# Optimization experiments

Measured on AMD Instinct MI355X. Metric: run time of the kernel, lower is better.

## Reference

```python
import jax, jax.numpy as jnp
import numpy as np

EPS = 1e-5
K_GROUP = 8  # k_group_size


def setup_inputs() -> dict:
    key = jax.random.key(0)
    ks = jax.random.split(key, 8)
    C = 384  # encoder_channel
    rn = lambda k, s: (jax.random.normal(k, s, dtype=jnp.float32) * 0.05)
    return {
        "point_groups": jax.random.normal(ks[0], (4, 256, 32, 3), dtype=jnp.float32),
        # first_conv: Conv1d(3,128,1)+BN+ReLU+Conv1d(128,256,1)
        "W1": rn(ks[1], (128, 3)), "b1": jnp.zeros(128, jnp.float32),
        "gamma1": jnp.ones(128, jnp.float32), "beta1": jnp.zeros(128, jnp.float32),
        "W2": rn(ks[2], (256, 128)), "b2": jnp.zeros(256, jnp.float32),
        # second_conv: Conv1d(512,512,1)+BN+ReLU+Conv1d(512,C,1)
        "W3": rn(ks[3], (512, 512)), "b3": jnp.zeros(512, jnp.float32),
        "gamma3": jnp.ones(512, jnp.float32), "beta3": jnp.zeros(512, jnp.float32),
        "W4": rn(ks[4], (C, 512)), "b4": jnp.zeros(C, jnp.float32),
        # K_Norm affine (out_dim = C, matching declared parameter shapes)
        "alpha": jnp.ones((1, 1, 1, C), jnp.float32),
        "beta_aff": jnp.zeros((1, 1, 1, C), jnp.float32),
        # fusion_layer: Conv1d(2C,C,1)+BN+ReLU
        "Wf": rn(ks[5], (C, 2 * C)), "bf": jnp.zeros(C, jnp.float32),
        "gammaf": jnp.ones(C, jnp.float32), "betaf": jnp.zeros(C, jnp.float32),
    }


def _conv1x1(x, W, b):  # x: (B,Cin,L), W: (Cout,Cin)
    return jnp.einsum("bcl,oc->bol", x, W) + b[None, :, None]


def _bn(x, gamma, beta):  # training-mode BatchNorm1d over (batch, length)
    mu = jnp.mean(x, axis=(0, 2), keepdims=True)
    var = jnp.var(x, axis=(0, 2), keepdims=True)
    xh = (x - mu) * jax.lax.rsqrt(var + EPS)
    return xh * gamma[None, :, None] + beta[None, :, None]


def reference(point_groups, W1, b1, gamma1, beta1, W2, b2, W3, b3, gamma3, beta3,
              W4, b4, alpha, beta_aff, Wf, bf, gammaf, betaf):
    bs, g, n, _ = point_groups.shape
    C = W4.shape[0]
    pg = point_groups.reshape(bs * g, n, 3)  # (B', n, 3)

    # first_conv stack
    f = _conv1x1(pg.transpose(0, 2, 1), W1, b1)           # (B',128,n)
    f = jax.nn.relu(_bn(f, gamma1, beta1))
    f = _conv1x1(f, W2, b2)                               # (B',256,n)
    fg = jnp.max(f, axis=2, keepdims=True)                # (B',256,1)
    f = jnp.concatenate([jnp.broadcast_to(fg, f.shape), f], axis=1)  # (B',512,n)

    # second_conv stack
    f = _conv1x1(f, W3, b3)
    f = jax.nn.relu(_bn(f, gamma3, beta3))
    f = _conv1x1(f, W4, b4)                               # (B',C,n)
    feat = f.transpose(0, 2, 1)                           # (B',n,C)

    # KNN within each group (self included, as in KNN(xyz,xyz))
    sq = jnp.sum(pg * pg, axis=-1)                        # (B',n)
    d = sq[:, :, None] + sq[:, None, :] - 2.0 * jnp.einsum("bnc,bmc->bnm", pg, pg)
    _, idx = jax.lax.top_k(-d, K_GROUP)                   # (B',n,K)

    gather = jax.vmap(lambda a, i: a[i])
    knn_x = gather(feat, idx)                             # (B',n,K,C)

    # K_Norm: center-relative normalization by global scalar std (torch.std, ddof=1)
    mean_x = feat[:, :, None, :]
    dx = knn_x - mean_x
    std_x = jnp.std(dx, ddof=1)
    knn_x = dx / (std_x + EPS)
    knn_x = alpha * knn_x + beta_aff                      # (B',n,K,C)

    enhanced = jnp.mean(knn_x, axis=2)                    # mean over K -> (B',n,C)
    enhanced = jnp.mean(enhanced, axis=1)                 # pool over n -> (B',C)

    fg2 = jnp.max(f, axis=2)                              # (B',C)
    fused_in = jnp.concatenate([fg2, enhanced], axis=1)[:, :, None]  # (B',2C,1)
    fused = jax.nn.relu(_bn(_conv1x1(fused_in, Wf, bf), gammaf, betaf))[:, :, 0]
    return fused.reshape(bs, g, C)
```

## Files before the change

### kernel.cpp

```cpp
#include <hip/hip_runtime.h>
#include <math.h>

#define EPS 1e-5f

typedef __attribute__((ext_vector_type(8))) short s16x8;
typedef __attribute__((ext_vector_type(4))) float f32x4;

__device__ __forceinline__ unsigned short f2bf(float x) {
    unsigned u = __float_as_uint(x);
    u += 0x7fffu + ((u >> 16) & 1u);
    return (unsigned short)(u >> 16);
}
__device__ __forceinline__ float bf2f(unsigned short h) {
    return __uint_as_float(((unsigned)h) << 16);
}
__device__ __forceinline__ unsigned long long pack4bf(float a, float b, float c, float d) {
    return (unsigned long long)f2bf(a)
         | ((unsigned long long)f2bf(b) << 16)
         | ((unsigned long long)f2bf(c) << 32)
         | ((unsigned long long)f2bf(d) << 48);
}

template<int CTRL>
__device__ __forceinline__ float dppmov(float x) {
    return __int_as_float(__builtin_amdgcn_update_dpp(
        0, __float_as_int(x), CTRL, 0xF, 0xF, true));
}
__device__ __forceinline__ float red16_sum(float x) {
    x += dppmov<0xB1>(x);
    x += dppmov<0x4E>(x);
    x += dppmov<0x141>(x);
    x += dppmov<0x140>(x);
    return x;
}
__device__ __forceinline__ float red16_max(float x) {
    x = fmaxf(x, dppmov<0xB1>(x));
    x = fmaxf(x, dppmov<0x4E>(x));
    x = fmaxf(x, dppmov<0x141>(x));
    x = fmaxf(x, dppmov<0x140>(x));
    return x;
}

__global__ __launch_bounds__(128) void k1_conv1_knn(
    const float* __restrict__ pg, const float* __restrict__ W1,
    const float* __restrict__ b1,
    const float* __restrict__ W2, const float* __restrict__ W3,
    const float* __restrict__ W4, const float* __restrict__ Wf,
    unsigned short* __restrict__ h1b, float* __restrict__ p1s, float* __restrict__ p1q,
    int* __restrict__ idxw,
    unsigned short* __restrict__ W2b, unsigned short* __restrict__ W3b,
    unsigned short* __restrict__ W4b, unsigned short* __restrict__ Wfb)
{
    __shared__ float pgs[96];
    __shared__ float sqs[32];
    if (blockIdx.x >= 1024) {
        const int i = (blockIdx.x - 1024) * 128 + threadIdx.x;
        if (i < 32768)  W2b[i] = f2bf(W2[i]);
        if (i < 262144) W3b[i] = f2bf(W3[i]);
        if (i < 196608) W4b[i] = f2bf(W4[i]);
        if (i < 294912) Wfb[i] = f2bf(Wf[i]);
        return;
    }
    const int b = blockIdx.x;
    const int t = threadIdx.x;
    if (t < 96) pgs[t] = pg[b * 96 + t];
    __syncthreads();
    if (t < 32) {
        float x = pgs[t*3+0], y = pgs[t*3+1], z = pgs[t*3+2];
        sqs[t] = x*x + y*y + z*z;
    }
    __syncthreads();
    {
        const float w0 = W1[t*3+0], w1 = W1[t*3+1], w2 = W1[t*3+2];
        const float bb = b1[t];
        float s = 0.f, q = 0.f;
        unsigned short* hcol = h1b + (size_t)b*4096 + t;
        #pragma unroll
        for (int l = 0; l < 32; ++l) {
            float v = fmaf(w2, pgs[l*3+2], fmaf(w1, pgs[l*3+1], fmaf(w0, pgs[l*3+0], bb)));
            hcol[l*128] = f2bf(v); s += v; q += v*v;
        }
        p1s[b*128 + t] = s;
        p1q[b*128 + t] = q;
    }
    if (t < 32) {
        const float xl = pgs[t*3+0], yl = pgs[t*3+1], zl = pgs[t*3+2];
        const float sql = sqs[t];
        float dist[32];
        #pragma unroll
        for (int m = 0; m < 32; ++m) {
            float dot = xl*pgs[m*3+0] + yl*pgs[m*3+1] + zl*pgs[m*3+2];
            dist[m] = sql + sqs[m] - 2.f*dot;
        }
        unsigned used = 0u;
        int* orow = idxw + b*256 + t*8;
        #pragma unroll
        for (int j = 0; j < 8; ++j) {
            float best = 3.4e38f; int bi = 0;
            #pragma unroll
            for (int m = 0; m < 32; ++m) {
                if (!((used >> m) & 1u) && dist[m] < best) { best = dist[m]; bi = m; }
            }
            used |= (1u << bi);
            orow[j] = bi;
        }
    }
}

__global__ __launch_bounds__(256) void k_bn_fin2(
    const float* __restrict__ ps, const float* __restrict__ pq,
    int nPart, int nChan, float invN,
    const float* __restrict__ gamma, const float* __restrict__ beta,
    float* __restrict__ scale, float* __restrict__ shift)
{
    const int ob = blockIdx.x * 4;
    const int t = threadIdx.x;
    const int co = t & 3, i0 = t >> 2;
    float s = 0.f, q = 0.f;
    for (int i = i0; i < nPart; i += 64) {
        s += ps[(size_t)i*nChan + ob + co];
        q += pq[(size_t)i*nChan + ob + co];
    }
    #pragma unroll
    for (int off = 32; off >= 4; off >>= 1) {
        s += __shfl_down(s, off, 64);
        q += __shfl_down(q, off, 64);
    }
    __shared__ float ss[4][4], qs[4][4];
    const int wid = t >> 6, lane = t & 63;
    if (lane < 4) { ss[wid][lane] = s; qs[wid][lane] = q; }
    __syncthreads();
    if (t < 4) {
        float S = ss[0][t] + ss[1][t] + ss[2][t] + ss[3][t];
        float Q = qs[0][t] + qs[1][t] + qs[2][t] + qs[3][t];
        const int o = ob + t;
        float mu  = S * invN;
        float var = Q * invN - mu*mu;
        float sc  = gamma[o] * rsqrtf(var + EPS);
        scale[o] = sc;
        shift[o] = beta[o] - mu * sc;
    }
}

__global__ __launch_bounds__(512, 4) void k3_mfma(
    const unsigned short* __restrict__ h1b,
    const float* __restrict__ scale1, const float* __restrict__ shift1,
    const unsigned short* __restrict__ W2b, const float* __restrict__ b2,
    const unsigned short* __restrict__ W3b, const float* __restrict__ b3,
    unsigned short* __restrict__ h3b, float* __restrict__ p3s, float* __restrict__ p3q)
{
    const int g0 = blockIdx.x * 2;
    const int t = threadIdx.x;
    __shared__ __align__(16) unsigned short SB[26128];
    unsigned short* B1  = SB;
    unsigned short* F2  = SB + 8704;
    unsigned short* FGB = SB + 25600;

    {
        const int l = t >> 3, c0 = (t & 7) * 16;
        const int g = g0 + (l >> 5);
        #pragma unroll
        for (int h = 0; h < 2; ++h) {
            s16x8 hv = *(const s16x8*)(h1b + (size_t)g*4096 + (l & 31)*128 + c0 + h*8);
            unsigned short ov[8];
            #pragma unroll
            for (int e = 0; e < 8; ++e) {
                int c = c0 + h*8 + e;
                float v = fmaxf(fmaf(bf2f((unsigned short)hv[e]), scale1[c], shift1[c]), 0.f);
                ov[e] = f2bf(v);
            }
            uint4 o4;
            o4.x = (unsigned)ov[0] | ((unsigned)ov[1] << 16);
            o4.y = (unsigned)ov[2] | ((unsigned)ov[3] << 16);
            o4.z = (unsigned)ov[4] | ((unsigned)ov[5] << 16);
            o4.w = (unsigned)ov[6] | ((unsigned)ov[7] << 16);
            *(uint4*)&B1[l*136 + c0 + h*8] = o4;
        }
    }
    __syncthreads();

    const int wave = t >> 6;
    const int lane = t & 63;
    const int m    = lane & 15;
    const int quad = lane >> 4;

    f32x4 acc2[2][4];
    #pragma unroll
    for (int mt = 0; mt < 2; ++mt)
        #pragma unroll
        for (int n = 0; n < 4; ++n)
            acc2[mt][n] = (f32x4){0.f, 0.f, 0.f, 0.f};

    #pragma unroll
    for (int kt = 0; kt < 4; ++kt) {
        s16x8 bv[4];
        #pragma unroll
        for (int nt = 0; nt < 4; ++nt)
            bv[nt] = *(const s16x8*)&B1[(nt*16 + m)*136 + kt*32 + quad*8];
        #pragma unroll
        for (int mt = 0; mt < 2; ++mt) {
            s16x8 av = *(const s16x8*)(W2b + (size_t)(wave*32 + mt*16 + m)*128 + kt*32 + quad*8);
            #pragma unroll
            for (int nt = 0; nt < 4; ++nt)
                acc2[mt][nt] = __builtin_amdgcn_mfma_f32_16x16x32_bf16(av, bv[nt], acc2[mt][nt], 0, 0, 0);
        }
    }

    #pragma unroll
    for (int mt = 0; mt < 2; ++mt) {
        const int o0 = wave*32 + mt*16 + quad*4;
        #pragma unroll
        for (int r = 0; r < 4; ++r) {
            float bb = b2[o0 + r];
            #pragma unroll
            for (int nt = 0; nt < 4; ++nt) acc2[mt][nt][r] += bb;
        }
        #pragma unroll
        for (int nt = 0; nt < 4; ++nt) {
            const int row = nt*16 + m;
            *(unsigned long long*)&F2[row*264 + o0] =
                pack4bf(acc2[mt][nt][0], acc2[mt][nt][1], acc2[mt][nt][2], acc2[mt][nt][3]);
        }
        float f0[4], f1[4];
        #pragma unroll
        for (int r = 0; r < 4; ++r) {
            f0[r] = red16_max(fmaxf(acc2[mt][0][r], acc2[mt][1][r]));
            f1[r] = red16_max(fmaxf(acc2[mt][2][r], acc2[mt][3][r]));
        }
        if (m == 0) {
            *(unsigned long long*)&FGB[o0]       = pack4bf(f0[0], f0[1], f0[2], f0[3]);
            *(unsigned long long*)&FGB[264 + o0] = pack4bf(f1[0], f1[1], f1[2], f1[3]);
        }
    }
    __syncthreads();

    f32x4 facc[4];
    #pragma unroll
    for (int i = 0; i < 4; ++i) facc[i] = (f32x4){0.f, 0.f, 0.f, 0.f};
    #pragma unroll
    for (int kt = 0; kt < 8; ++kt) {
        s16x8 bg = *(const s16x8*)&FGB[(m & 1)*264 + kt*32 + quad*8];
        #pragma unroll
        for (int i = 0; i < 4; ++i) {
            s16x8 av = *(const s16x8*)(W3b + (size_t)((wave*4 + i)*16 + m)*512 + kt*32 + quad*8);
            facc[i] = __builtin_amdgcn_mfma_f32_16x16x32_bf16(av, bg, facc[i], 0, 0, 0);
        }
    }

    f32x4 acc3[4][4];
    #pragma unroll
    for (int mt = 0; mt < 4; ++mt) {
        #pragma unroll
        for (int r = 0; r < 4; ++r) {
            const int ob = (wave*4 + mt)*16 + quad*4 + r;
            float self = facc[mt][r];
            float oth  = dppmov<0xB1>(self);
            float fg_g0 = (m & 1) ? oth : self;
            float fg_g1 = (m & 1) ? self : oth;
            float bb = b3[ob];
            acc3[mt][0][r] = bb + fg_g0;
            acc3[mt][1][r] = bb + fg_g0;
            acc3[mt][2][r] = bb + fg_g1;
            acc3[mt][3][r] = bb + fg_g1;
        }
    }
    #pragma unroll 4
    for (int kt = 0; kt < 8; ++kt) {
        s16x8 bv[4];
        #pragma unroll
        for (int nt = 0; nt < 4; ++nt)
            bv[nt] = *(const s16x8*)&F2[(nt*16 + m)*264 + kt*32 + quad*8];
        #pragma unroll
        for (int mt = 0; mt < 4; ++mt) {
            s16x8 av = *(const s16x8*)(W3b + (size_t)((wave*4 + mt)*16 + m)*512 + 256 + kt*32 + quad*8);
            #pragma unroll
            for (int nt = 0; nt < 4; ++nt)
                acc3[mt][nt] = __builtin_amdgcn_mfma_f32_16x16x32_bf16(av, bv[nt], acc3[mt][nt], 0, 0, 0);
        }
    }

    unsigned short* dst = h3b + (size_t)blockIdx.x * 32768;
    #pragma unroll
    for (int mt = 0; mt < 4; ++mt) {
        const int ot = wave*4 + mt;
        const int o0 = ot*16 + quad*4;
        float s[4], q[4];
        #pragma unroll
        for (int r = 0; r < 4; ++r) {
            float x0 = acc3[mt][0][r], x1 = acc3[mt][1][r];
            float x2 = acc3[mt][2][r], x3 = acc3[mt][3][r];
            s[r] = (x0 + x1) + (x2 + x3);
            q[r] = (x0*x0 + x1*x1) + (x2*x2 + x3*x3);
        }
        {
            unsigned long long u0 = pack4bf(acc3[mt][0][0], acc3[mt][0][1], acc3[mt][0][2], acc3[mt][0][3]);
            unsigned long long u1 = pack4bf(acc3[mt][1][0], acc3[mt][1][1], acc3[mt][1][2], acc3[mt][1][3]);
            unsigned long long u2 = pack4bf(acc3[mt][2][0], acc3[mt][2][1], acc3[mt][2][2], acc3[mt][2][3]);
            unsigned long long u3 = pack4bf(acc3[mt][3][0], acc3[mt][3][1], acc3[mt][3][2], acc3[mt][3][3]);
            unsigned short* p = dst + (size_t)(ot*64 + lane) * 16;
            *(uint4*)(p)     = make_uint4((unsigned)u0, (unsigned)(u0 >> 32), (unsigned)u1, (unsigned)(u1 >> 32));
            *(uint4*)(p + 8) = make_uint4((unsigned)u2, (unsigned)(u2 >> 32), (unsigned)u3, (unsigned)(u3 >> 32));
        }
        #pragma unroll
        for (int r = 0; r < 4; ++r) {
            s[r] = red16_sum(s[r]);
            q[r] = red16_sum(q[r]);
        }
        if (m == 0) {
            #pragma unroll
            for (int r = 0; r < 4; ++r) {
                p3s[(size_t)blockIdx.x*512 + o0 + r] = s[r];
                p3q[(size_t)blockIdx.x*512 + o0 + r] = q[r];
            }
        }
    }
}

__global__ __launch_bounds__(512, 4) void k5_mfma(
    const unsigned short* __restrict__ h3b,
    const float* __restrict__ scale3, const float* __restrict__ shift3,
    const unsigned short* __restrict__ W4b, const float* __restrict__ b4,
    const int* __restrict__ idxw,
    float* __restrict__ fg2, float* __restrict__ A,
    float* __restrict__ S1p, float* __restrict__ S2p)
{
    const int g0 = blockIdx.x * 2;
    const int t = threadIdx.x;
    __shared__ __align__(16) unsigned short SB[33280];
    unsigned short* B4 = SB;
    unsigned short* XT = SB;
    unsigned short* Mm = SB + 30720;
    __shared__ int icnt[2][32];
    __shared__ float r1[2][8], r2[2][8];

    {
        const uint4* src = (const uint4*)(h3b + (size_t)blockIdx.x * 32768);
        for (int i = t; i < 4096; i += 512) {
            uint4 hv = src[i];
            const int flat16 = i >> 1, half = i & 1;
            const int ln = flat16 & 63, m2 = ln & 15, q2 = ln >> 4;
            const int wm = flat16 >> 6;
            const int o0 = wm*16 + q2*4;
            const float4 sc = *(const float4*)(scale3 + o0);
            const float4 sh = *(const float4*)(shift3 + o0);
            const int rowa = (half*2)*16 + m2;
            float a0 = fmaxf(fmaf(bf2f((unsigned short)(hv.x       )), sc.x, sh.x), 0.f);
            float a1 = fmaxf(fmaf(bf2f((unsigned short)(hv.x >> 16 )), sc.y, sh.y), 0.f);
            float a2 = fmaxf(fmaf(bf2f((unsigned short)(hv.y       )), sc.z, sh.z), 0.f);
            float a3 = fmaxf(fmaf(bf2f((unsigned short)(hv.y >> 16 )), sc.w, sh.w), 0.f);
            float b0 = fmaxf(fmaf(bf2f((unsigned short)(hv.z       )), sc.x, sh.x), 0.f);
            float b1 = fmaxf(fmaf(bf2f((unsigned short)(hv.z >> 16 )), sc.y, sh.y), 0.f);
            float b2 = fmaxf(fmaf(bf2f((unsigned short)(hv.w       )), sc.z, sh.z), 0.f);
            float b3 = fmaxf(fmaf(bf2f((unsigned short)(hv.w >> 16 )), sc.w, sh.w), 0.f);
            *(unsigned long long*)&B4[rowa*520 + o0]        = pack4bf(a0, a1, a2, a3);
            *(unsigned long long*)&B4[(rowa + 16)*520 + o0] = pack4bf(b0, b1, b2, b3);
        }
    }
    if (t < 64) icnt[t >> 5][t & 31] = 0;
    __syncthreads();

    const int wave = t >> 6;
    const int lane = t & 63;
    const int m    = lane & 15;
    const int quad = lane >> 4;

    f32x4 acc4[3][4];
    #pragma unroll
    for (int mt = 0; mt < 3; ++mt)
        #pragma unroll
        for (int n = 0; n < 4; ++n)
            acc4[mt][n] = (f32x4){0.f, 0.f, 0.f, 0.f};

    #pragma unroll 4
    for (int kt = 0; kt < 16; ++kt) {
        s16x8 bv[4];
        #pragma unroll
        for (int nt = 0; nt < 4; ++nt)
            bv[nt] = *(const s16x8*)&B4[(nt*16 + m)*520 + kt*32 + quad*8];
        #pragma unroll
        for (int mt = 0; mt < 3; ++mt) {
            s16x8 av = *(const s16x8*)(W4b + (size_t)(wave*48 + mt*16 + m)*512 + kt*32 + quad*8);
            #pragma unroll
            for (int nt = 0; nt < 4; ++nt)
                acc4[mt][nt] = __builtin_amdgcn_mfma_f32_16x16x32_bf16(av, bv[nt], acc4[mt][nt], 0, 0, 0);
        }
    }

    #pragma unroll
    for (int mt = 0; mt < 3; ++mt) {
        const int o0 = wave*48 + mt*16 + quad*4;
        float f0[4], f1[4];
        #pragma unroll
        for (int r = 0; r < 4; ++r) {
            float bb = b4[o0 + r];
            #pragma unroll
            for (int nt = 0; nt < 4; ++nt) acc4[mt][nt][r] += bb;
            f0[r] = red16_max(fmaxf(acc4[mt][0][r], acc4[mt][1][r]));
            f1[r] = red16_max(fmaxf(acc4[mt][2][r], acc4[mt][3][r]));
        }
        if (m == 0) {
            #pragma unroll
            for (int r = 0; r < 4; ++r) {
                fg2[(size_t)g0*384 + o0 + r]     = f0[r];
                fg2[(size_t)(g0+1)*384 + o0 + r] = f1[r];
            }
        }
    }
    __syncthreads();

    #pragma unroll
    for (int mt = 0; mt < 3; ++mt) {
        const int o0 = wave*48 + mt*16 + quad*4;
        #pragma unroll
        for (int nt = 0; nt < 4; ++nt) {
            const int g = nt >> 1;
            const int l = (nt & 1)*16 + m;
            unsigned short* xg = XT + g*15360;
            #pragma unroll
            for (int r = 0; r < 4; ++r)
                xg[(o0 + r)*40 + l] = f2bf(acc4[mt][nt][r]);
        }
    }
    if (t < 64) {
        const int g = t >> 5, l = t & 31;
        uint4 z = make_uint4(0u, 0u, 0u, 0u);
        #pragma unroll
        for (int i = 0; i < 5; ++i)
            *(uint4*)&Mm[g*1280 + l*40 + i*8] = z;
    }
    __syncthreads();

    if (t < 64) {
        const int g = t >> 5, l = t & 31;
        const int* ip = idxw + (size_t)(g0 + g)*256 + l*8;
        #pragma unroll
        for (int j = 0; j < 8; ++j) {
            int ix = ip[j];
            Mm[g*1280 + l*40 + ix] = 0x3F80;
            atomicAdd(&icnt[g][ix], 1);
        }
    }
    __syncthreads();

    float s1loc[2] = {0.f, 0.f}, s2loc[2] = {0.f, 0.f};
    #pragma unroll
    for (int g = 0; g < 2; ++g) {
        const float c0 = (float)icnt[g][m];
        const float c1 = (float)icnt[g][m + 16];
        const float w0 = c0 - 8.f, u0 = c0 + 8.f;
        const float w1 = c1 - 8.f, u1 = c1 + 8.f;
        #pragma unroll
        for (int mt = 0; mt < 3; ++mt) {
            const int o0 = wave*48 + mt*16 + quad*4;
            float Ap[4];
            #pragma unroll
            for (int r = 0; r < 4; ++r) {
                const float x0 = acc4[mt][g*2 + 0][r];
                const float x1 = acc4[mt][g*2 + 1][r];
                Ap[r] = w0*x0 + w1*x1;
                s1loc[g] += Ap[r];
                s2loc[g] += u0*x0*x0 + u1*x1*x1;
            }
            #pragma unroll
            for (int r = 0; r < 4; ++r)
                Ap[r] = red16_sum(Ap[r]);
            if (m == 0) {
                #pragma unroll
                for (int r = 0; r < 4; ++r)
                    A[(size_t)(g0 + g)*384 + o0 + r] = Ap[r];
            }
        }
    }

    #pragma unroll
    for (int g = 0; g < 2; ++g) {
        const unsigned short* xg = XT + g*15360;
        float cross = 0.f;
        #pragma unroll
        for (int lt = 0; lt < 2; ++lt) {
            s16x8 af = *(const s16x8*)&Mm[g*1280 + (lt*16 + m)*40 + quad*8];
            #pragma unroll
            for (int i = 0; i < 3; ++i) {
                const int oc = (wave*3 + i)*16 + m;
                s16x8 bfv = *(const s16x8*)&xg[oc*40 + quad*8];
                f32x4 sa = __builtin_amdgcn_mfma_f32_16x16x32_bf16(
                    af, bfv, (f32x4){0.f, 0.f, 0.f, 0.f}, 0, 0, 0);
                #pragma unroll
                for (int r = 0; r < 4; ++r) {
                    const int lp = lt*16 + quad*4 + r;
                    cross = fmaf(bf2f(xg[oc*40 + lp]), sa[r], cross);
                }
            }
        }
        s2loc[g] -= 2.f * cross;
    }

    #pragma unroll
    for (int g = 0; g < 2; ++g) {
        float sA = s1loc[g], sQ = s2loc[g];
        #pragma unroll
        for (int off = 32; off > 0; off >>= 1) {
            sA += __shfl_down(sA, off, 64);
            sQ += __shfl_down(sQ, off, 64);
        }
        if (lane == 0) { r1[g][wave] = sA; r2[g][wave] = sQ; }
    }
    __syncthreads();
    if (t < 2) {
        float S = 0.f, Q = 0.f;
        #pragma unroll
        for (int w = 0; w < 8; ++w) { S += r1[t][w]; Q += r2[t][w]; }
        S1p[g0 + t] = S;
        S2p[g0 + t] = Q;
    }
}

__global__ __launch_bounds__(384) void k7_fused(
    const float* __restrict__ fg2, const float* __restrict__ A,
    const float* __restrict__ alpha, const float* __restrict__ beta_aff,
    const float* __restrict__ S1p, const float* __restrict__ S2p,
    const unsigned short* __restrict__ Wfb, const float* __restrict__ bf,
    float* __restrict__ hf, float* __restrict__ pfs, float* __restrict__ pfq)
{
    const int blk    = blockIdx.x;
    const int slice  = blk >> 2;
    const int msplit = blk & 3;
    const int g0     = slice * 16;
    const int obase  = msplit * 96;
    const int t = threadIdx.x;
    __shared__ __align__(16) char smem[24832];
    unsigned short* xfb = (unsigned short*)smem;
    float* OTf = (float*)smem;
    __shared__ double rs[6], rq[6];
    __shared__ float stdsh;

    {
        double s = 0.0, q = 0.0;
        for (int i = t; i < 1024; i += 384) { s += (double)S1p[i]; q += (double)S2p[i]; }
        #pragma unroll
        for (int off = 32; off > 0; off >>= 1) {
            s += __shfl_down(s, off, 64);
            q += __shfl_down(q, off, 64);
        }
        if ((t & 63) == 0) { rs[t >> 6] = s; rq[t >> 6] = q; }
        __syncthreads();
        if (t == 0) {
            double S = 0.0, Q = 0.0;
            #pragma unroll
            for (int w = 0; w < 6; ++w) { S += rs[w]; Q += rq[w]; }
            const double N = 1024.0 * 32.0 * 8.0 * 384.0;
            double var = (Q - S*S/N) / (N - 1.0);
            stdsh = (float)sqrt(var);
        }
        __syncthreads();
    }
    const float inv = 1.f / (256.f * (stdsh + EPS));

    for (int i = t; i < 16*96; i += 384) {
        const int row = i / 96, c8 = (i % 96) * 8;
        const int g = g0 + row;
        float e[8];
        if (c8 < 384) {
            const float4* s0 = (const float4*)(fg2 + (size_t)g*384 + c8);
            float4 v0 = s0[0], v1 = s0[1];
            e[0]=v0.x; e[1]=v0.y; e[2]=v0.z; e[3]=v0.w;
            e[4]=v1.x; e[5]=v1.y; e[6]=v1.z; e[7]=v1.w;
        } else {
            const int cc = c8 - 384;
            const float4* s0 = (const float4*)(A + (size_t)g*384 + cc);
            float4 v0 = s0[0], v1 = s0[1];
            float av[8] = {v0.x,v0.y,v0.z,v0.w,v1.x,v1.y,v1.z,v1.w};
            #pragma unroll
            for (int j = 0; j < 8; ++j)
                e[j] = fmaf(alpha[cc+j] * inv, av[j], beta_aff[cc+j]);
        }
        uint4 o4;
        o4.x = (unsigned)f2bf(e[0]) | ((unsigned)f2bf(e[1]) << 16);
        o4.y = (unsigned)f2bf(e[2]) | ((unsigned)f2bf(e[3]) << 16);
        o4.z = (unsigned)f2bf(e[4]) | ((unsigned)f2bf(e[5]) << 16);
        o4.w = (unsigned)f2bf(e[6]) | ((unsigned)f2bf(e[7]) << 16);
        *(uint4*)&xfb[row*776 + c8] = o4;
    }
    __syncthreads();

    const int wave = t >> 6;
    const int lane = t & 63;
    const int m    = lane & 15;
    const int quad = lane >> 4;

    f32x4 acc = (f32x4){0.f, 0.f, 0.f, 0.f};
    #pragma unroll 4
    for (int kt = 0; kt < 24; ++kt) {
        s16x8 bv = *(const s16x8*)&xfb[m*776 + kt*32 + quad*8];
        s16x8 av = *(const s16x8*)(Wfb + (size_t)(obase + wave*16 + m)*768 + kt*32 + quad*8);
        acc = __builtin_amdgcn_mfma_f32_16x16x32_bf16(av, bv, acc, 0, 0, 0);
    }

    {
        const int o0 = obase + wave*16 + quad*4;
        float s[4], q[4];
        #pragma unroll
        for (int r = 0; r < 4; ++r) {
            acc[r] += bf[o0 + r];
            s[r] = red16_sum(acc[r]);
            q[r] = red16_sum(acc[r]*acc[r]);
        }
        if (m == 0) {
            #pragma unroll
            for (int r = 0; r < 4; ++r) {
                pfs[(size_t)slice*384 + o0 + r] = s[r];
                pfq[(size_t)slice*384 + o0 + r] = q[r];
            }
        }
    }
    __syncthreads();

    {
        const int lo0 = wave*16 + quad*4;
        #pragma unroll
        for (int r = 0; r < 4; ++r)
            OTf[m*100 + lo0 + r] = acc[r];
    }
    __syncthreads();

    {
        const int grp = t / 24, c4 = t % 24;
        float4 v = *(const float4*)&OTf[grp*100 + c4*4];
        *(float4*)(hf + (size_t)(g0 + grp)*384 + obase + c4*4) = v;
    }
}

__global__ __launch_bounds__(384) void k9_out(
    const float* __restrict__ hf,
    const float* __restrict__ pfs, const float* __restrict__ pfq,
    const float* __restrict__ gammaf, const float* __restrict__ betaf,
    float* __restrict__ out)
{
    const int blk = blockIdx.x, t = threadIdx.x;
    float S = 0.f, Q = 0.f;
    #pragma unroll 8
    for (int i = 0; i < 64; ++i) {
        S += pfs[(size_t)i*384 + t];
        Q += pfq[(size_t)i*384 + t];
    }
    const float mu  = S * (1.f/1024.f);
    const float var = Q * (1.f/1024.f) - mu*mu;
    const float sc  = gammaf[t] * rsqrtf(var + EPS);
    const float sh  = betaf[t] - mu * sc;
    const size_t base = (size_t)blk * 8 * 384;
    #pragma unroll
    for (int g = 0; g < 8; ++g) {
        float v = fmaf(hf[base + g*384 + t], sc, sh);
        out[base + g*384 + t] = fmaxf(v, 0.f);
    }
}

extern "C" void kernel_launch(void* const* d_in, const int* in_sizes, int n_in,
                              void* d_out, int out_size, void* d_ws, size_t ws_size,
                              hipStream_t stream) {
    const float* pg      = (const float*)d_in[0];
    const float* W1      = (const float*)d_in[1];
    const float* b1      = (const float*)d_in[2];
    const float* gamma1  = (const float*)d_in[3];
    const float* beta1   = (const float*)d_in[4];
    const float* W2      = (const float*)d_in[5];
    const float* b2      = (const float*)d_in[6];
    const float* W3      = (const float*)d_in[7];
    const float* b3      = (const float*)d_in[8];
    const float* gamma3  = (const float*)d_in[9];
    const float* beta3   = (const float*)d_in[10];
    const float* W4      = (const float*)d_in[11];
    const float* b4      = (const float*)d_in[12];
    const float* alpha   = (const float*)d_in[13];
    const float* beta_af = (const float*)d_in[14];
    const float* Wf      = (const float*)d_in[15];
    const float* bf      = (const float*)d_in[16];
    const float* gammaf  = (const float*)d_in[17];
    const float* betaf   = (const float*)d_in[18];
    float* out = (float*)d_out;

    float* w = (float*)d_ws;
    unsigned short* h1b = (unsigned short*)w; w += 1024*4096/2;
    unsigned short* h3b = (unsigned short*)w; w += 1024*16384/2;
    unsigned short* W2b = (unsigned short*)w; w += 32768/2;
    unsigned short* W3b = (unsigned short*)w; w += 262144/2;
    unsigned short* W4b = (unsigned short*)w; w += 196608/2;
    unsigned short* Wfb = (unsigned short*)w; w += 294912/2;
    float* hf     = w;  w += 1024*384;
    float* fg2    = w;  w += 1024*384;
    float* A      = w;  w += 1024*384;
    float* p1s    = w;  w += 1024*128;
    float* p1q    = w;  w += 1024*128;
    float* p3s    = w;  w += 1024*512;
    float* p3q    = w;  w += 1024*512;
    float* pfs    = w;  w += 64*384;
    float* pfq    = w;  w += 64*384;
    float* S1p    = w;  w += 1024;
    float* S2p    = w;  w += 1024;
    float* scale1 = w;  w += 128;
    float* shift1 = w;  w += 128;
    float* scale3 = w;  w += 512;
    float* shift3 = w;  w += 512;
    int*   idxw   = (int*)w;  w += 1024*256;

    hipLaunchKernelGGL(k1_conv1_knn, dim3(1024 + 2304), dim3(128), 0, stream,
                       pg, W1, b1, W2, W3, W4, Wf,
                       h1b, p1s, p1q, idxw, W2b, W3b, W4b, Wfb);
    hipLaunchKernelGGL(k_bn_fin2, dim3(32), dim3(256), 0, stream,
                       p1s, p1q, 1024, 128, 1.f/32768.f, gamma1, beta1, scale1, shift1);
    hipLaunchKernelGGL(k3_mfma, dim3(512), dim3(512), 0, stream,
                       h1b, scale1, shift1, W2b, b2, W3b, b3, h3b, p3s, p3q);
    hipLaunchKernelGGL(k_bn_fin2, dim3(128), dim3(256), 0, stream,
                       p3s, p3q, 512, 512, 1.f/32768.f, gamma3, beta3, scale3, shift3);
    hipLaunchKernelGGL(k5_mfma, dim3(512), dim3(512), 0, stream,
                       h3b, scale3, shift3, W4b, b4, idxw, fg2, A, S1p, S2p);
    hipLaunchKernelGGL(k7_fused, dim3(256), dim3(384), 0, stream,
                       fg2, A, alpha, beta_af, S1p, S2p, Wfb, bf, hf, pfs, pfq);
    hipLaunchKernelGGL(k9_out, dim3(128), dim3(384), 0, stream,
                       hf, pfs, pfq, gammaf, betaf, out);
}
```

Measured before the change: 207.9 us.

## Process W3 output tiles one at a time to cut accumulator registers

Restructures the second-conv GEMM so each wave handles one 16-row output tile at a time. For each tile it computes the global-feature contribution, the main MFMA loop over K and the stats/store epilogue before moving on, instead of holding all 4x4 accumulator tiles live at once. The aim is to reduce VGPR/AGPR pressure so occupancy can rise. In exchange, the F2 B-fragments in LDS are re-read once per output tile (4x more LDS traffic), and there is less MFMA independence to hide latency.

```diff
diff --git a/kernel.cpp b/kernel.cpp
--- a/kernel.cpp
+++ b/kernel.cpp
@@ -234,69 +234,59 @@
     }
     __syncthreads();
 
-    f32x4 facc[4];
-    #pragma unroll
-    for (int i = 0; i < 4; ++i) facc[i] = (f32x4){0.f, 0.f, 0.f, 0.f};
-    #pragma unroll
-    for (int kt = 0; kt < 8; ++kt) {
-        s16x8 bg = *(const s16x8*)&FGB[(m & 1)*264 + kt*32 + quad*8];
-        #pragma unroll
-        for (int i = 0; i < 4; ++i) {
-            s16x8 av = *(const s16x8*)(W3b + (size_t)((wave*4 + i)*16 + m)*512 + kt*32 + quad*8);
-            facc[i] = __builtin_amdgcn_mfma_f32_16x16x32_bf16(av, bg, facc[i], 0, 0, 0);
-        }
-    }
-
-    f32x4 acc3[4][4];
+    unsigned short* dst = h3b + (size_t)blockIdx.x * 32768;
     #pragma unroll
     for (int mt = 0; mt < 4; ++mt) {
+        const int ot = wave*4 + mt;
+        const int o0 = ot*16 + quad*4;
+
+        f32x4 facc = (f32x4){0.f, 0.f, 0.f, 0.f};
+        #pragma unroll
+        for (int kt = 0; kt < 8; ++kt) {
+            s16x8 bg = *(const s16x8*)&FGB[(m & 1)*264 + kt*32 + quad*8];
+            s16x8 av = *(const s16x8*)(W3b + (size_t)(ot*16 + m)*512 + kt*32 + quad*8);
+            facc = __builtin_amdgcn_mfma_f32_16x16x32_bf16(av, bg, facc, 0, 0, 0);
+        }
+
+        f32x4 acc3[4];
         #pragma unroll
         for (int r = 0; r < 4; ++r) {
-            const int ob = (wave*4 + mt)*16 + quad*4 + r;
-            float self = facc[mt][r];
+            float self = facc[r];
             float oth  = dppmov<0xB1>(self);
             float fg_g0 = (m & 1) ? oth : self;
             float fg_g1 = (m & 1) ? self : oth;
-            float bb = b3[ob];
-            acc3[mt][0][r] = bb + fg_g0;
-            acc3[mt][1][r] = bb + fg_g0;
-            acc3[mt][2][r] = bb + fg_g1;
-            acc3[mt][3][r] = bb + fg_g1;
-        }
-    }
-    #pragma unroll 4
-    for (int kt = 0; kt < 8; ++kt) {
-        s16x8 bv[4];
-        #pragma unroll
-        for (int nt = 0; nt < 4; ++nt)
-            bv[nt] = *(const s16x8*)&F2[(nt*16 + m)*264 + kt*32 + quad*8];
-        #pragma unroll
-        for (int mt = 0; mt < 4; ++mt) {
-            s16x8 av = *(const s16x8*)(W3b + (size_t)((wave*4 + mt)*16 + m)*512 + 256 + kt*32 + quad*8);
+            float bb = b3[o0 + r];
+            acc3[0][r] = bb + fg_g0;
+            acc3[1][r] = bb + fg_g0;
+            acc3[2][r] = bb + fg_g1;
+            acc3[3][r] = bb + fg_g1;
+        }
+
+        #pragma unroll
+        for (int kt = 0; kt < 8; ++kt) {
+            s16x8 bv[4];
             #pragma unroll
             for (int nt = 0; nt < 4; ++nt)
-                acc3[mt][nt] = __builtin_amdgcn_mfma_f32_16x16x32_bf16(av, bv[nt], acc3[mt][nt], 0, 0, 0);
-        }
-    }
-
-    unsigned short* dst = h3b + (size_t)blockIdx.x * 32768;
-    #pragma unroll
-    for (int mt = 0; mt < 4; ++mt) {
-        const int ot = wave*4 + mt;
-        const int o0 = ot*16 + quad*4;
+                bv[nt] = *(const s16x8*)&F2[(nt*16 + m)*264 + kt*32 + quad*8];
+            s16x8 av = *(const s16x8*)(W3b + (size_t)(ot*16 + m)*512 + 256 + kt*32 + quad*8);
+            #pragma unroll
+            for (int nt = 0; nt < 4; ++nt)
+                acc3[nt] = __builtin_amdgcn_mfma_f32_16x16x32_bf16(av, bv[nt], acc3[nt], 0, 0, 0);
+        }
+
         float s[4], q[4];
         #pragma unroll
         for (int r = 0; r < 4; ++r) {
-            float x0 = acc3[mt][0][r], x1 = acc3[mt][1][r];
-            float x2 = acc3[mt][2][r], x3 = acc3[mt][3][r];
+            float x0 = acc3[0][r], x1 = acc3[1][r];
+            float x2 = acc3[2][r], x3 = acc3[3][r];
             s[r] = (x0 + x1) + (x2 + x3);
             q[r] = (x0*x0 + x1*x1) + (x2*x2 + x3*x3);
         }
         {
-            unsigned long long u0 = pack4bf(acc3[mt][0][0], acc3[mt][0][1], acc3[mt][0][2], acc3[mt][0][3]);
-            unsigned long long u1 = pack4bf(acc3[mt][1][0], acc3[mt][1][1], acc3[mt][1][2], acc3[mt][1][3]);
-            unsigned long long u2 = pack4bf(acc3[mt][2][0], acc3[mt][2][1], acc3[mt][2][2], acc3[mt][2][3]);
-            unsigned long long u3 = pack4bf(acc3[mt][3][0], acc3[mt][3][1], acc3[mt][3][2], acc3[mt][3][3]);
+            unsigned long long u0 = pack4bf(acc3[0][0], acc3[0][1], acc3[0][2], acc3[0][3]);
+            unsigned long long u1 = pack4bf(acc3[1][0], acc3[1][1], acc3[1][2], acc3[1][3]);
+            unsigned long long u2 = pack4bf(acc3[2][0], acc3[2][1], acc3[2][2], acc3[2][3]);
+            unsigned long long u3 = pack4bf(acc3[3][0], acc3[3][1], acc3[3][2], acc3[3][3]);
             unsigned short* p = dst + (size_t)(ot*64 + lane) * 16;
             *(uint4*)(p)     = make_uint4((unsigned)u0, (unsigned)(u0 >> 32), (unsigned)u1, (unsigned)(u1 >> 32));
             *(uint4*)(p + 8) = make_uint4((unsigned)u2, (unsigned)(u2 >> 32), (unsigned)u3, (unsigned)(u3 >> 32));
```

Result: no change. 208.3 us (+0.2%).
